# Kernel tuning notes

Hardware: AMD Instinct MI355X
Metric: run time of the kernel (lower is better)

## Reference

```python
import jax, jax.numpy as jnp
import numpy as np

B, N, C, H, W = 2, 6, 256, 56, 100
Q, E, NH = 900, 256, 8
EPS = 1e-5


def setup_inputs() -> dict:
    key = jax.random.key(0)
    ks = jax.random.split(key, 20)
    s = 0.02
    return {
        "image_features": jax.random.normal(ks[0], (B, N, C, H, W), jnp.float32),
        "lidar2img": jax.random.normal(ks[1], (B, N, 4, 4), jnp.float32),
        "query_table": jax.random.normal(ks[2], (Q, E), jnp.float32) * s,
        "ref_W": jax.random.normal(ks[3], (E, 3), jnp.float32) * s,
        "ref_b": jnp.zeros((3,), jnp.float32),
        "Wq": jax.random.normal(ks[4], (E, E), jnp.float32) * s,
        "bq": jnp.zeros((E,), jnp.float32),
        "Wk": jax.random.normal(ks[5], (E, E), jnp.float32) * s,
        "bk": jnp.zeros((E,), jnp.float32),
        "Wv": jax.random.normal(ks[6], (E, E), jnp.float32) * s,
        "bv": jnp.zeros((E,), jnp.float32),
        "Wo": jax.random.normal(ks[7], (E, E), jnp.float32) * s,
        "bo": jnp.zeros((E,), jnp.float32),
        "ln_g": jnp.ones((E,), jnp.float32),
        "ln_b": jnp.zeros((E,), jnp.float32),
        "box_W": jax.random.normal(ks[8], (E, 10), jnp.float32) * s,
        "box_b": jnp.zeros((10,), jnp.float32),
    }


def _grid_sample_bilinear(feats, grid):
    # feats: (M,C,H,W); grid: (M,P,2) in [-1,1]; align_corners=False, zero padding
    M, Cc, Hh, Ww = feats.shape
    gx, gy = grid[..., 0], grid[..., 1]
    x = ((gx + 1.0) * Ww - 1.0) * 0.5
    y = ((gy + 1.0) * Hh - 1.0) * 0.5
    x0 = jnp.floor(x); y0 = jnp.floor(y)
    wx1 = x - x0; wx0 = 1.0 - wx1
    wy1 = y - y0; wy0 = 1.0 - wy1
    midx = jnp.arange(M)[:, None]

    def gather(xi, yi):
        inb = (xi >= 0) & (xi < Ww) & (yi >= 0) & (yi < Hh)
        xi_c = jnp.clip(xi, 0, Ww - 1).astype(jnp.int32)
        yi_c = jnp.clip(yi, 0, Hh - 1).astype(jnp.int32)
        vals = feats[midx, :, yi_c, xi_c]  # (M,P,C)
        return vals * inb[..., None].astype(feats.dtype)

    out = (gather(x0, y0) * (wx0 * wy0)[..., None]
           + gather(x0 + 1, y0) * (wx1 * wy0)[..., None]
           + gather(x0, y0 + 1) * (wx0 * wy1)[..., None]
           + gather(x0 + 1, y0 + 1) * (wx1 * wy1)[..., None])
    return out  # (M,P,C)


def _layer_norm(x, g, b):
    mu = jnp.mean(x, -1, keepdims=True)
    var = jnp.mean((x - mu) ** 2, -1, keepdims=True)
    return (x - mu) * jax.lax.rsqrt(var + EPS) * g + b


def _forward(image_features, lidar2img, query_table, ref_W, ref_b,
             Wq, bq, Wk, bk, Wv, bv, Wo, bo, ln_g, ln_b, box_W, box_b):
    Bv = image_features.shape[0]
    qe = jnp.broadcast_to(query_table[None], (Bv, Q, E))  # (B,Q,E)

    # Step 1: reference points
    ref3d = jax.nn.sigmoid(qe @ ref_W + ref_b)  # (B,Q,3)

    # Step 2: project 3D -> 2D
    pts_h = jnp.concatenate([ref3d, jnp.ones_like(ref3d[..., :1])], -1)  # (B,Q,4)
    p2h = jnp.einsum('bnij,bqj->bnqi', lidar2img, pts_h)  # (B,N,Q,4)
    z = p2h[..., 2:3]
    pts2d = p2h[..., 0:2] / (jnp.abs(z) + 1e-5)  # (B,N,Q,2)
    zmask = (z > 1e-5)[..., 0]  # (B,N,Q)

    # Step 3: normalize + grid_sample + masked average
    gx = pts2d[..., 0] / (W - 1) * 2.0 - 1.0
    gy = pts2d[..., 1] / (H - 1) * 2.0 - 1.0
    grid = jnp.stack([gx, gy], -1).reshape(Bv * N, Q, 2)
    feats = image_features.reshape(Bv * N, C, H, W)
    samp = _grid_sample_bilinear(feats, grid).reshape(Bv, N, Q, C)
    samp = jnp.transpose(samp, (0, 2, 1, 3))  # (B,Q,N,C)

    valid = (gx > -1) & (gx < 1) & (gy > -1) & (gy < 1)  # (B,N,Q)
    final_mask = (zmask & valid).transpose(0, 2, 1)[..., None]  # (B,Q,N,1)
    samp = samp * final_mask.astype(samp.dtype)
    count = jnp.clip(final_mask.sum(2), 1, None).astype(samp.dtype)  # (B,Q,1)
    tgt = samp.sum(2) / count  # (B,Q,C)

    x = qe + tgt

    # self-attention (torch MultiheadAttention math)
    hd = E // NH
    q = (x @ Wq + bq).reshape(Bv, Q, NH, hd)
    k = (x @ Wk + bk).reshape(Bv, Q, NH, hd)
    v = (x @ Wv + bv).reshape(Bv, Q, NH, hd)
    att = jnp.einsum('bqhd,bkhd->bhqk', q, k) / jnp.sqrt(jnp.float32(hd))
    att = jax.nn.softmax(att, -1)
    o = jnp.einsum('bhqk,bkhd->bqhd', att, v).reshape(Bv, Q, E)
    x = o @ Wo + bo

    out = _layer_norm(x, ln_g, ln_b) @ box_W + box_b  # (B,Q,10)
    return out, ref3d


def reference(image_features, lidar2img, query_table, ref_W, ref_b,
              Wq, bq, Wk, bk, Wv, bv, Wo, bo, ln_g, ln_b, box_W, box_b):
    return _forward(image_features, lidar2img, query_table, ref_W, ref_b,
                    Wq, bq, Wk, bk, Wv, bv, Wo, bo, ln_g, ln_b, box_W, box_b)
```

## Files before the change

### kernel.cpp

```cpp
#include <hip/hip_runtime.h>
#include <math.h>

static constexpr int Bv  = 2;
static constexpr int Ncam= 6;
static constexpr int Cch = 256;
static constexpr int Hh  = 56;
static constexpr int Ww  = 100;
static constexpr int Pn  = Hh * Ww;
static constexpr int Qn  = 900;
static constexpr int En  = 256;
static constexpr int NH  = 8;
static constexpr int HD  = 32;

typedef _Float16 f16x8 __attribute__((ext_vector_type(8)));
typedef _Float16 f16x4 __attribute__((ext_vector_type(4)));
typedef float    f32x4 __attribute__((ext_vector_type(4)));

__global__ void wpack_kernel(const float* __restrict__ W0,
                             const float* __restrict__ W1,
                             const float* __restrict__ W2,
                             const float* __restrict__ W3,
                             _Float16* __restrict__ outp) {
    __shared__ float tile[32][33];
    int z = blockIdx.z;
    const float* src = (z == 0) ? W0 : (z == 1) ? W1 : (z == 2) ? W2 : W3;
    int k0 = blockIdx.x * 32, n0 = blockIdx.y * 32;
    int tx = threadIdx.x, ty = threadIdx.y;
    for (int i = 0; i < 32; i += 8)
        tile[ty + i][tx] = src[(size_t)(k0 + ty + i) * 256 + n0 + tx];
    __syncthreads();
    _Float16* dst = outp + (size_t)z * 256 * 256;
    for (int i = 0; i < 32; i += 8)
        dst[(size_t)(n0 + ty + i) * 256 + k0 + tx] = (_Float16)tile[tx][ty + i];
}

__global__ void ref_grid_kernel(const float* __restrict__ qt,
                                const float* __restrict__ refW,
                                const float* __restrict__ refb,
                                const float* __restrict__ l2i,
                                float* __restrict__ gridbuf,
                                float* __restrict__ out_ref3d) {
    int q = blockIdx.x;
    int t = threadIdx.x;
    float s0 = 0.f, s1 = 0.f, s2 = 0.f;
    for (int i = t; i < En; i += 64) {
        float a = qt[q * En + i];
        s0 += a * refW[i * 3 + 0];
        s1 += a * refW[i * 3 + 1];
        s2 += a * refW[i * 3 + 2];
    }
    for (int off = 32; off > 0; off >>= 1) {
        s0 += __shfl_down(s0, off);
        s1 += __shfl_down(s1, off);
        s2 += __shfl_down(s2, off);
    }
    __shared__ float r3[3];
    if (t == 0) {
        float v0 = 1.f / (1.f + expf(-(s0 + refb[0])));
        float v1 = 1.f / (1.f + expf(-(s1 + refb[1])));
        float v2 = 1.f / (1.f + expf(-(s2 + refb[2])));
        r3[0] = v0; r3[1] = v1; r3[2] = v2;
        out_ref3d[(size_t)(0 * Qn + q) * 3 + 0] = v0;
        out_ref3d[(size_t)(0 * Qn + q) * 3 + 1] = v1;
        out_ref3d[(size_t)(0 * Qn + q) * 3 + 2] = v2;
        out_ref3d[(size_t)(1 * Qn + q) * 3 + 0] = v0;
        out_ref3d[(size_t)(1 * Qn + q) * 3 + 1] = v1;
        out_ref3d[(size_t)(1 * Qn + q) * 3 + 2] = v2;
    }
    __syncthreads();
    if (t < Bv * Ncam) {
        int b = t / Ncam, n = t % Ncam;
        const float* M = l2i + (size_t)(b * Ncam + n) * 16;
        float p0 = M[0] * r3[0] + M[1] * r3[1] + M[2]  * r3[2] + M[3];
        float p1 = M[4] * r3[0] + M[5] * r3[1] + M[6]  * r3[2] + M[7];
        float z  = M[8] * r3[0] + M[9] * r3[1] + M[10] * r3[2] + M[11];
        float denom = fabsf(z) + 1e-5f;
        float px = p0 / denom, py = p1 / denom;
        float gx = px / (float)(Ww - 1) * 2.f - 1.f;
        float gy = py / (float)(Hh - 1) * 2.f - 1.f;
        bool zm = z > 1e-5f;
        bool valid = (gx > -1.f) && (gx < 1.f) && (gy > -1.f) && (gy < 1.f);
        float* g = gridbuf + ((size_t)(b * Ncam + n) * Qn + q) * 3;
        g[0] = gx; g[1] = gy; g[2] = (zm && valid) ? 1.f : 0.f;
    }
}

__global__ __launch_bounds__(256)
void feat_pack_kernel(const float* __restrict__ in, _Float16* __restrict__ outp) {
    __shared__ _Float16 tile[32][132];
    int m = blockIdx.z;
    int p0 = blockIdx.x * 128, c0 = blockIdx.y * 32;
    int t = threadIdx.x;
    {
        int p4 = (t & 31) * 4;
        int cc0 = t >> 5;
        for (int i = 0; i < 4; i++) {
            int cc = cc0 + i * 8;
            int p = p0 + p4;
            if (p < Pn) {
                float4 v = *(const float4*)&in[((size_t)m * Cch + c0 + cc) * Pn + p];
                f16x4 h = {(_Float16)v.x, (_Float16)v.y, (_Float16)v.z, (_Float16)v.w};
                *(f16x4*)&tile[cc][p4] = h;
            }
        }
    }
    __syncthreads();
    {
        int cg = (t & 7) * 4;
        int pr = t >> 3;
        for (int i = 0; i < 4; i++) {
            int pl = pr + i * 32;
            int p = p0 + pl;
            if (p < Pn) {
                f16x4 h = {tile[0][0], tile[0][0], tile[0][0], tile[0][0]};
                h.x = tile[cg + 0][pl];
                h.y = tile[cg + 1][pl];
                h.z = tile[cg + 2][pl];
                h.w = tile[cg + 3][pl];
                *(f16x4*)&outp[((size_t)m * Pn + p) * Cch + c0 + cg] = h;
            }
        }
    }
}

__device__ __forceinline__ float corner_val(const _Float16* __restrict__ base,
                                            int xi, int yi, int c) {
    if (xi < 0 || xi >= Ww || yi < 0 || yi >= Hh) return 0.f;
    return (float)base[((size_t)yi * Ww + xi) * Cch + c];
}

__global__ void sample_kernel(const _Float16* __restrict__ featsT,
                              const float* __restrict__ gridbuf,
                              const float* __restrict__ qt,
                              _Float16* __restrict__ xbuf) {
    int bq = blockIdx.x;
    int b = bq / Qn, q = bq % Qn;
    int c = threadIdx.x;
    float acc = 0.f, cnt = 0.f;
    for (int n = 0; n < Ncam; n++) {
        const float* g = gridbuf + ((size_t)(b * Ncam + n) * Qn + q) * 3;
        float gx = g[0], gy = g[1], msk = g[2];
        if (msk > 0.5f) {
            cnt += 1.f;
            float x = ((gx + 1.f) * (float)Ww - 1.f) * 0.5f;
            float y = ((gy + 1.f) * (float)Hh - 1.f) * 0.5f;
            float x0f = floorf(x), y0f = floorf(y);
            int x0 = (int)x0f, y0 = (int)y0f;
            float wx1 = x - x0f, wx0 = 1.f - wx1;
            float wy1 = y - y0f, wy0 = 1.f - wy1;
            int m = b * Ncam + n;
            const _Float16* base = featsT + (size_t)m * Pn * Cch;
            acc += corner_val(base, x0,     y0,     c) * (wx0 * wy0);
            acc += corner_val(base, x0 + 1, y0,     c) * (wx1 * wy0);
            acc += corner_val(base, x0,     y0 + 1, c) * (wx0 * wy1);
            acc += corner_val(base, x0 + 1, y0 + 1, c) * (wx1 * wy1);
        }
    }
    float tgt = acc / fmaxf(cnt, 1.f);
    xbuf[(size_t)bq * En + c] = (_Float16)(qt[q * En + c] + tgt);
}

__device__ __forceinline__ void mfma_gemm_body(const _Float16* __restrict__ A,
                                               const _Float16* __restrict__ Wt,
                                               const float* __restrict__ bias,
                                               _Float16* __restrict__ Cf16,
                                               float* __restrict__ Cf32,
                                               int M, int m0, int n0) {
    __shared__ _Float16 Ws[64][264];
    int t = threadIdx.x;
    int wave = t >> 6, lane = t & 63, quad = lane >> 4, col = lane & 15;
    {
        int row = t >> 5;
        int off = (t & 31) * 8;
        for (int i = 0; i < 8; i++)
            *(f16x8*)&Ws[row + i * 8][off] =
                *(const f16x8*)&Wt[(size_t)(n0 + row + i * 8) * 256 + off];
    }
    f16x8 af[8];
    int mrow = m0 + wave * 16 + col;
    if (mrow < M) {
        const _Float16* ap = A + (size_t)mrow * 256 + quad * 8;
        #pragma unroll
        for (int kc = 0; kc < 8; kc++) af[kc] = *(const f16x8*)(ap + kc * 32);
    } else {
        #pragma unroll
        for (int kc = 0; kc < 8; kc++)
            #pragma unroll
            for (int j = 0; j < 8; j++) af[kc][j] = (_Float16)0.f;
    }
    __syncthreads();
    f32x4 acc[4];
    #pragma unroll
    for (int nt = 0; nt < 4; nt++) { acc[nt][0]=0.f; acc[nt][1]=0.f; acc[nt][2]=0.f; acc[nt][3]=0.f; }
    #pragma unroll
    for (int nt = 0; nt < 4; nt++)
        #pragma unroll
        for (int kc = 0; kc < 8; kc++) {
            f16x8 bf = *(const f16x8*)&Ws[nt * 16 + col][kc * 32 + quad * 8];
            acc[nt] = __builtin_amdgcn_mfma_f32_16x16x32_f16(af[kc], bf, acc[nt], 0, 0, 0);
        }
    #pragma unroll
    for (int nt = 0; nt < 4; nt++) {
        int n = n0 + nt * 16 + col;
        float bv = bias[n];
        #pragma unroll
        for (int r = 0; r < 4; r++) {
            int m = m0 + wave * 16 + quad * 4 + r;
            if (m < M) {
                float v = acc[nt][r] + bv;
                if (Cf16) Cf16[(size_t)m * 256 + n] = (_Float16)v;
                else      Cf32[(size_t)m * 256 + n] = v;
            }
        }
    }
}

__global__ __launch_bounds__(256)
void qkv_mfma_kernel(const _Float16* __restrict__ A,
                     const _Float16* __restrict__ Wtall,
                     const float* __restrict__ bq, const float* __restrict__ bk,
                     const float* __restrict__ bv,
                     _Float16* __restrict__ qo, _Float16* __restrict__ ko,
                     _Float16* __restrict__ vo, int M) {
    const _Float16* Wt; const float* bias; _Float16* out;
    if (blockIdx.z == 0)      { Wt = Wtall;               bias = bq; out = qo; }
    else if (blockIdx.z == 1) { Wt = Wtall + 256 * 256;   bias = bk; out = ko; }
    else                      { Wt = Wtall + 2 * 256 * 256; bias = bv; out = vo; }
    mfma_gemm_body(A, Wt, bias, out, nullptr, M, blockIdx.x * 64, blockIdx.y * 64);
}

__global__ __launch_bounds__(256)
void wo_mfma_kernel(const _Float16* __restrict__ A,
                    const _Float16* __restrict__ Wtall,
                    const float* __restrict__ bo,
                    float* __restrict__ x2, int M) {
    mfma_gemm_body(A, Wtall + 3 * 256 * 256, bo, nullptr, x2, M,
                   blockIdx.x * 64, blockIdx.y * 64);
}

static constexpr int FTQ = 64;
static constexpr int FTK = 64;

__global__ __launch_bounds__(256)
void flash_attn_mfma_kernel(const _Float16* __restrict__ qbuf,
                            const _Float16* __restrict__ kbuf,
                            const _Float16* __restrict__ vbuf,
                            _Float16* __restrict__ obuf) {
    __shared__ _Float16 Ks[FTK][40];
    __shared__ _Float16 Vt[HD][72];
    __shared__ _Float16 Ps[4][16][72];

    int bh = blockIdx.y;
    int b = bh / NH, h = bh % NH;
    int m0 = blockIdx.x * FTQ;
    int t = threadIdx.x;
    int wave = t >> 6, lane = t & 63;
    int quad = lane >> 4, col = lane & 15;

    const float scale = 0.17677669529663687f;

    f16x8 qf;
    {
        int qrow = m0 + wave * 16 + col;
        if (qrow < Qn) {
            qf = *(const f16x8*)(qbuf + ((size_t)b * Qn + qrow) * En + h * HD + quad * 8);
        } else {
            #pragma unroll
            for (int j = 0; j < 8; j++) qf[j] = (_Float16)0.f;
        }
    }

    f32x4 o0 = {0.f, 0.f, 0.f, 0.f};
    f32x4 o1 = {0.f, 0.f, 0.f, 0.f};
    float mrow[4] = {-3e38f, -3e38f, -3e38f, -3e38f};
    float lrow[4] = {0.f, 0.f, 0.f, 0.f};

    int nstage = t >> 2;
    int kk4 = (t & 3) * 8;

    for (int n0 = 0; n0 < Qn; n0 += FTK) {
        {
            int ng = n0 + nstage;
            f16x8 kb, vb;
            if (ng < Qn) {
                kb = *(const f16x8*)(kbuf + ((size_t)b * Qn + ng) * En + h * HD + kk4);
                vb = *(const f16x8*)(vbuf + ((size_t)b * Qn + ng) * En + h * HD + kk4);
            } else {
                #pragma unroll
                for (int j = 0; j < 8; j++) { kb[j] = (_Float16)0.f; vb[j] = (_Float16)0.f; }
            }
            *(f16x8*)&Ks[nstage][kk4] = kb;
            #pragma unroll
            for (int j = 0; j < 8; j++) Vt[kk4 + j][nstage] = vb[j];
        }
        __syncthreads();

        f32x4 S[4];
        #pragma unroll
        for (int c = 0; c < 4; c++) {
            f16x8 kf = *(const f16x8*)&Ks[c * 16 + col][quad * 8];
            f32x4 z = {0.f, 0.f, 0.f, 0.f};
            S[c] = __builtin_amdgcn_mfma_f32_16x16x32_f16(qf, kf, z, 0, 0, 0);
            S[c] *= scale;
        }
        if (n0 + FTK > Qn) {
            #pragma unroll
            for (int c = 0; c < 4; c++) {
                if (n0 + c * 16 + col >= Qn) {
                    S[c][0] = -3e38f; S[c][1] = -3e38f; S[c][2] = -3e38f; S[c][3] = -3e38f;
                }
            }
        }

        float p[4][4];
        #pragma unroll
        for (int r = 0; r < 4; r++) {
            float mx = fmaxf(fmaxf(S[0][r], S[1][r]), fmaxf(S[2][r], S[3][r]));
            #pragma unroll
            for (int off = 8; off >= 1; off >>= 1)
                mx = fmaxf(mx, __shfl_xor(mx, off, 64));
            float mnew = fmaxf(mrow[r], mx);
            float alpha = __expf(mrow[r] - mnew);
            mrow[r] = mnew;
            float rs = 0.f;
            #pragma unroll
            for (int c = 0; c < 4; c++) {
                float pv = __expf(S[c][r] - mnew);
                p[c][r] = pv;
                rs += pv;
            }
            #pragma unroll
            for (int off = 8; off >= 1; off >>= 1)
                rs += __shfl_xor(rs, off, 64);
            lrow[r] = lrow[r] * alpha + rs;
            o0[r] *= alpha;
            o1[r] *= alpha;
        }

        #pragma unroll
        for (int c = 0; c < 4; c++)
            #pragma unroll
            for (int r = 0; r < 4; r++)
                Ps[wave][quad * 4 + r][c * 16 + col] = (_Float16)p[c][r];

        #pragma unroll
        for (int kc = 0; kc < 2; kc++) {
            f16x8 pf = *(const f16x8*)&Ps[wave][col][kc * 32 + quad * 8];
            f16x8 v0 = *(const f16x8*)&Vt[col][kc * 32 + quad * 8];
            f16x8 v1 = *(const f16x8*)&Vt[16 + col][kc * 32 + quad * 8];
            o0 = __builtin_amdgcn_mfma_f32_16x16x32_f16(pf, v0, o0, 0, 0, 0);
            o1 = __builtin_amdgcn_mfma_f32_16x16x32_f16(pf, v1, o1, 0, 0, 0);
        }
        __syncthreads();
    }

    #pragma unroll
    for (int r = 0; r < 4; r++) {
        int q = m0 + wave * 16 + quad * 4 + r;
        if (q < Qn) {
            float inv = 1.f / lrow[r];
            _Float16* op = obuf + ((size_t)b * Qn + q) * En + h * HD;
            op[col]      = (_Float16)(o0[r] * inv);
            op[16 + col] = (_Float16)(o1[r] * inv);
        }
    }
}

__global__ void ln_box_kernel(const float* __restrict__ x2,
                              const float* __restrict__ ln_g,
                              const float* __restrict__ ln_b,
                              const float* __restrict__ boxW,
                              const float* __restrict__ boxb,
                              float* __restrict__ outp) {
    __shared__ float red[256];
    __shared__ float yrow[En];
    __shared__ float pbox[16][10];
    int bq = blockIdx.x;
    int t = threadIdx.x;
    float acc = x2[(size_t)bq * En + t];
    red[t] = acc; __syncthreads();
    for (int s = 128; s > 0; s >>= 1) {
        if (t < s) red[t] += red[t + s];
        __syncthreads();
    }
    float mu = red[0] / (float)En;
    __syncthreads();
    float dx = acc - mu;
    red[t] = dx * dx; __syncthreads();
    for (int s = 128; s > 0; s >>= 1) {
        if (t < s) red[t] += red[t + s];
        __syncthreads();
    }
    float var = red[0] / (float)En;
    float y = dx * rsqrtf(var + 1e-5f) * ln_g[t] + ln_b[t];
    yrow[t] = y;
    __syncthreads();
    if (t < 160) {
        int j = t % 10, ch = t / 10;
        float p = 0.f;
        for (int k = ch * 16; k < ch * 16 + 16; k++)
            p += yrow[k] * boxW[(size_t)k * 10 + j];
        pbox[ch][j] = p;
    }
    __syncthreads();
    if (t < 10) {
        float o = boxb[t];
        for (int ch = 0; ch < 16; ch++) o += pbox[ch][t];
        outp[(size_t)bq * 10 + t] = o;
    }
}

extern "C" void kernel_launch(void* const* d_in, const int* in_sizes, int n_in,
                              void* d_out, int out_size, void* d_ws, size_t ws_size,
                              hipStream_t stream) {
    const float* image_features = (const float*)d_in[0];
    const float* lidar2img      = (const float*)d_in[1];
    const float* query_table    = (const float*)d_in[2];
    const float* ref_W          = (const float*)d_in[3];
    const float* ref_b          = (const float*)d_in[4];
    const float* Wq             = (const float*)d_in[5];
    const float* bq             = (const float*)d_in[6];
    const float* Wk             = (const float*)d_in[7];
    const float* bk             = (const float*)d_in[8];
    const float* Wv             = (const float*)d_in[9];
    const float* bv             = (const float*)d_in[10];
    const float* Wo             = (const float*)d_in[11];
    const float* bo             = (const float*)d_in[12];
    const float* ln_g           = (const float*)d_in[13];
    const float* ln_b           = (const float*)d_in[14];
    const float* box_W          = (const float*)d_in[15];
    const float* box_b          = (const float*)d_in[16];
    float* out = (float*)d_out;

    char* ws = (char*)d_ws;
    size_t off = 0;
    auto alloc = [&](size_t bytes) { char* p = ws + off; off += (bytes + 255) & ~size_t(255); return p; };
    float*     gridbuf = (float*)    alloc((size_t)Bv * Ncam * Qn * 3 * 4);
    _Float16*  featsT  = (_Float16*) alloc((size_t)Bv * Ncam * Pn * Cch * 2);
    _Float16*  xbuf    = (_Float16*) alloc((size_t)Bv * Qn * En * 2);
    _Float16*  qbuf    = (_Float16*) alloc((size_t)Bv * Qn * En * 2);
    _Float16*  kbuf    = (_Float16*) alloc((size_t)Bv * Qn * En * 2);
    _Float16*  vbuf    = (_Float16*) alloc((size_t)Bv * Qn * En * 2);
    _Float16*  obuf    = (_Float16*) alloc((size_t)Bv * Qn * En * 2);
    float*     x2buf   = (float*)    alloc((size_t)Bv * Qn * En * 4);
    _Float16*  Wtall   = (_Float16*) alloc((size_t)4 * 256 * 256 * 2);

    float* out_ref3d = out + (size_t)Bv * Qn * 10;
    int M = Bv * Qn;

    hipLaunchKernelGGL(wpack_kernel, dim3(8, 8, 4), dim3(32, 8), 0, stream,
                       Wq, Wk, Wv, Wo, Wtall);

    hipLaunchKernelGGL(ref_grid_kernel, dim3(Qn), dim3(64), 0, stream,
                       query_table, ref_W, ref_b, lidar2img, gridbuf, out_ref3d);

    hipLaunchKernelGGL(feat_pack_kernel,
                       dim3((Pn + 127) / 128, Cch / 32, Bv * Ncam), dim3(256),
                       0, stream, image_features, featsT);

    hipLaunchKernelGGL(sample_kernel, dim3(Bv * Qn), dim3(256), 0, stream,
                       featsT, gridbuf, query_table, xbuf);

    hipLaunchKernelGGL(qkv_mfma_kernel, dim3((M + 63) / 64, En / 64, 3), dim3(256),
                       0, stream, xbuf, Wtall, bq, bk, bv, qbuf, kbuf, vbuf, M);

    hipLaunchKernelGGL(flash_attn_mfma_kernel,
                       dim3((Qn + FTQ - 1) / FTQ, Bv * NH), dim3(256), 0, stream,
                       qbuf, kbuf, vbuf, obuf);

    hipLaunchKernelGGL(wo_mfma_kernel, dim3((M + 63) / 64, En / 64), dim3(256),
                       0, stream, obuf, Wtall, bo, x2buf, M);

    hipLaunchKernelGGL(ln_box_kernel, dim3(Bv * Qn), dim3(256), 0, stream,
                       x2buf, ln_g, ln_b, box_W, box_b, out);
}
```

Before: 185.0 us.

## Fuse prelude kernels, Wo GEMM with LayerNorm/box head; widen attention K tile

```diff
diff --git a/kernel.cpp b/kernel.cpp
--- a/kernel.cpp
+++ b/kernel.cpp
@@ -14,74 +14,72 @@
 
 typedef _Float16 f16x8 __attribute__((ext_vector_type(8)));
 typedef _Float16 f16x4 __attribute__((ext_vector_type(4)));
+typedef _Float16 f16x2 __attribute__((ext_vector_type(2)));
 typedef float    f32x4 __attribute__((ext_vector_type(4)));
 
-__global__ void wpack_kernel(const float* __restrict__ W0,
-                             const float* __restrict__ W1,
-                             const float* __restrict__ W2,
-                             const float* __restrict__ W3,
-                             _Float16* __restrict__ outp) {
-    __shared__ float tile[32][33];
-    int z = blockIdx.z;
-    const float* src = (z == 0) ? W0 : (z == 1) ? W1 : (z == 2) ? W2 : W3;
-    int k0 = blockIdx.x * 32, n0 = blockIdx.y * 32;
-    int tx = threadIdx.x, ty = threadIdx.y;
-    for (int i = 0; i < 32; i += 8)
-        tile[ty + i][tx] = src[(size_t)(k0 + ty + i) * 256 + n0 + tx];
-    __syncthreads();
-    _Float16* dst = outp + (size_t)z * 256 * 256;
-    for (int i = 0; i < 32; i += 8)
-        dst[(size_t)(n0 + ty + i) * 256 + k0 + tx] = (_Float16)tile[tx][ty + i];
-}
-
-__global__ void ref_grid_kernel(const float* __restrict__ qt,
-                                const float* __restrict__ refW,
-                                const float* __restrict__ refb,
-                                const float* __restrict__ l2i,
-                                float* __restrict__ gridbuf,
-                                float* __restrict__ out_ref3d) {
-    int q = blockIdx.x;
+__global__ __launch_bounds__(256)
+void prelude_kernel(const float* __restrict__ W0, const float* __restrict__ W1,
+                    const float* __restrict__ W2, const float* __restrict__ W3,
+                    _Float16* __restrict__ wt_out,
+                    const float* __restrict__ qt, const float* __restrict__ refW,
+                    const float* __restrict__ refb, const float* __restrict__ l2i,
+                    float* __restrict__ gridbuf, float* __restrict__ out_ref3d) {
+    int bid = blockIdx.x;
     int t = threadIdx.x;
-    float s0 = 0.f, s1 = 0.f, s2 = 0.f;
-    for (int i = t; i < En; i += 64) {
-        float a = qt[q * En + i];
-        s0 += a * refW[i * 3 + 0];
-        s1 += a * refW[i * 3 + 1];
-        s2 += a * refW[i * 3 + 2];
-    }
-    for (int off = 32; off > 0; off >>= 1) {
-        s0 += __shfl_down(s0, off);
-        s1 += __shfl_down(s1, off);
-        s2 += __shfl_down(s2, off);
-    }
-    __shared__ float r3[3];
-    if (t == 0) {
-        float v0 = 1.f / (1.f + expf(-(s0 + refb[0])));
-        float v1 = 1.f / (1.f + expf(-(s1 + refb[1])));
-        float v2 = 1.f / (1.f + expf(-(s2 + refb[2])));
-        r3[0] = v0; r3[1] = v1; r3[2] = v2;
-        out_ref3d[(size_t)(0 * Qn + q) * 3 + 0] = v0;
-        out_ref3d[(size_t)(0 * Qn + q) * 3 + 1] = v1;
-        out_ref3d[(size_t)(0 * Qn + q) * 3 + 2] = v2;
-        out_ref3d[(size_t)(1 * Qn + q) * 3 + 0] = v0;
-        out_ref3d[(size_t)(1 * Qn + q) * 3 + 1] = v1;
-        out_ref3d[(size_t)(1 * Qn + q) * 3 + 2] = v2;
-    }
-    __syncthreads();
-    if (t < Bv * Ncam) {
-        int b = t / Ncam, n = t % Ncam;
-        const float* M = l2i + (size_t)(b * Ncam + n) * 16;
-        float p0 = M[0] * r3[0] + M[1] * r3[1] + M[2]  * r3[2] + M[3];
-        float p1 = M[4] * r3[0] + M[5] * r3[1] + M[6]  * r3[2] + M[7];
-        float z  = M[8] * r3[0] + M[9] * r3[1] + M[10] * r3[2] + M[11];
-        float denom = fabsf(z) + 1e-5f;
-        float px = p0 / denom, py = p1 / denom;
-        float gx = px / (float)(Ww - 1) * 2.f - 1.f;
-        float gy = py / (float)(Hh - 1) * 2.f - 1.f;
-        bool zm = z > 1e-5f;
-        bool valid = (gx > -1.f) && (gx < 1.f) && (gy > -1.f) && (gy < 1.f);
-        float* g = gridbuf + ((size_t)(b * Ncam + n) * Qn + q) * 3;
-        g[0] = gx; g[1] = gy; g[2] = (zm && valid) ? 1.f : 0.f;
+    if (bid < 256) {
+        __shared__ float tile[32][33];
+        int z = bid >> 6, rem = bid & 63;
+        const float* src = (z == 0) ? W0 : (z == 1) ? W1 : (z == 2) ? W2 : W3;
+        int k0 = (rem & 7) * 32, n0 = (rem >> 3) * 32;
+        int tx = t & 31, ty = t >> 5;
+        for (int i = 0; i < 32; i += 8)
+            tile[ty + i][tx] = src[(size_t)(k0 + ty + i) * 256 + n0 + tx];
+        __syncthreads();
+        _Float16* dst = wt_out + (size_t)z * 256 * 256;
+        for (int i = 0; i < 32; i += 8)
+            dst[(size_t)(n0 + ty + i) * 256 + k0 + tx] = (_Float16)tile[tx][ty + i];
+    } else {
+        int wave = t >> 6, lane = t & 63;
+        int q = (bid - 256) * 4 + wave;
+        float s0 = 0.f, s1 = 0.f, s2 = 0.f;
+        for (int i = lane; i < En; i += 64) {
+            float a = qt[q * En + i];
+            s0 += a * refW[i * 3 + 0];
+            s1 += a * refW[i * 3 + 1];
+            s2 += a * refW[i * 3 + 2];
+        }
+        for (int off = 32; off > 0; off >>= 1) {
+            s0 += __shfl_down(s0, off);
+            s1 += __shfl_down(s1, off);
+            s2 += __shfl_down(s2, off);
+        }
+        s0 = __shfl(s0, 0); s1 = __shfl(s1, 0); s2 = __shfl(s2, 0);
+        float v0 = 1.f / (1.f + __expf(-(s0 + refb[0])));
+        float v1 = 1.f / (1.f + __expf(-(s1 + refb[1])));
+        float v2 = 1.f / (1.f + __expf(-(s2 + refb[2])));
+        if (lane == 0) {
+            out_ref3d[(size_t)q * 3 + 0] = v0;
+            out_ref3d[(size_t)q * 3 + 1] = v1;
+            out_ref3d[(size_t)q * 3 + 2] = v2;
+            out_ref3d[(size_t)(Qn + q) * 3 + 0] = v0;
+            out_ref3d[(size_t)(Qn + q) * 3 + 1] = v1;
+            out_ref3d[(size_t)(Qn + q) * 3 + 2] = v2;
+        }
+        if (lane < Bv * Ncam) {
+            int b = lane / Ncam, n = lane % Ncam;
+            const float* M = l2i + (size_t)(b * Ncam + n) * 16;
+            float p0 = M[0] * v0 + M[1] * v1 + M[2]  * v2 + M[3];
+            float p1 = M[4] * v0 + M[5] * v1 + M[6]  * v2 + M[7];
+            float z  = M[8] * v0 + M[9] * v1 + M[10] * v2 + M[11];
+            float denom = fabsf(z) + 1e-5f;
+            float px = p0 / denom, py = p1 / denom;
+            float gx = px / (float)(Ww - 1) * 2.f - 1.f;
+            float gy = py / (float)(Hh - 1) * 2.f - 1.f;
+            bool zm = z > 1e-5f;
+            bool valid = (gx > -1.f) && (gx < 1.f) && (gy > -1.f) && (gy < 1.f);
+            float* g = gridbuf + ((size_t)(b * Ncam + n) * Qn + q) * 3;
+            g[0] = gx; g[1] = gy; g[2] = (zm && valid) ? 1.f : 0.f;
+        }
     }
 }
 
@@ -112,7 +110,7 @@
             int pl = pr + i * 32;
             int p = p0 + pl;
             if (p < Pn) {
-                f16x4 h = {tile[0][0], tile[0][0], tile[0][0], tile[0][0]};
+                f16x4 h;
                 h.x = tile[cg + 0][pl];
                 h.y = tile[cg + 1][pl];
                 h.z = tile[cg + 2][pl];
@@ -123,20 +121,25 @@
     }
 }
 
-__device__ __forceinline__ float corner_val(const _Float16* __restrict__ base,
-                                            int xi, int yi, int c) {
-    if (xi < 0 || xi >= Ww || yi < 0 || yi >= Hh) return 0.f;
-    return (float)base[((size_t)yi * Ww + xi) * Cch + c];
-}
-
-__global__ void sample_kernel(const _Float16* __restrict__ featsT,
-                              const float* __restrict__ gridbuf,
-                              const float* __restrict__ qt,
-                              _Float16* __restrict__ xbuf) {
-    int bq = blockIdx.x;
+__device__ __forceinline__ void corner_acc2(const _Float16* __restrict__ base,
+                                            int xi, int yi, int ch, float w,
+                                            float& a0, float& a1) {
+    if (xi < 0 || xi >= Ww || yi < 0 || yi >= Hh) return;
+    f16x2 v = *(const f16x2*)&base[((size_t)yi * Ww + xi) * Cch + ch];
+    a0 += (float)v.x * w;
+    a1 += (float)v.y * w;
+}
+
+__global__ __launch_bounds__(256)
+void sample_kernel(const _Float16* __restrict__ featsT,
+                   const float* __restrict__ gridbuf,
+                   const float* __restrict__ qt,
+                   _Float16* __restrict__ xbuf) {
+    int t = threadIdx.x;
+    int bq = blockIdx.x * 2 + (t >> 7);
     int b = bq / Qn, q = bq % Qn;
-    int c = threadIdx.x;
-    float acc = 0.f, cnt = 0.f;
+    int ch = (t & 127) * 2;
+    float a0 = 0.f, a1 = 0.f, cnt = 0.f;
     for (int n = 0; n < Ncam; n++) {
         const float* g = gridbuf + ((size_t)(b * Ncam + n) * Qn + q) * 3;
         float gx = g[0], gy = g[1], msk = g[2];
@@ -148,23 +151,25 @@
             int x0 = (int)x0f, y0 = (int)y0f;
             float wx1 = x - x0f, wx0 = 1.f - wx1;
             float wy1 = y - y0f, wy0 = 1.f - wy1;
-            int m = b * Ncam + n;
-            const _Float16* base = featsT + (size_t)m * Pn * Cch;
-            acc += corner_val(base, x0,     y0,     c) * (wx0 * wy0);
-            acc += corner_val(base, x0 + 1, y0,     c) * (wx1 * wy0);
-            acc += corner_val(base, x0,     y0 + 1, c) * (wx0 * wy1);
-            acc += corner_val(base, x0 + 1, y0 + 1, c) * (wx1 * wy1);
-        }
-    }
-    float tgt = acc / fmaxf(cnt, 1.f);
-    xbuf[(size_t)bq * En + c] = (_Float16)(qt[q * En + c] + tgt);
+            const _Float16* base = featsT + (size_t)(b * Ncam + n) * Pn * Cch;
+            corner_acc2(base, x0,     y0,     ch, wx0 * wy0, a0, a1);
+            corner_acc2(base, x0 + 1, y0,     ch, wx1 * wy0, a0, a1);
+            corner_acc2(base, x0,     y0 + 1, ch, wx0 * wy1, a0, a1);
+            corner_acc2(base, x0 + 1, y0 + 1, ch, wx1 * wy1, a0, a1);
+        }
+    }
+    float inv = 1.f / fmaxf(cnt, 1.f);
+    float2 qv = *(const float2*)&qt[(size_t)q * En + ch];
+    f16x2 o;
+    o.x = (_Float16)(qv.x + a0 * inv);
+    o.y = (_Float16)(qv.y + a1 * inv);
+    *(f16x2*)&xbuf[(size_t)bq * En + ch] = o;
 }
 
 __device__ __forceinline__ void mfma_gemm_body(const _Float16* __restrict__ A,
                                                const _Float16* __restrict__ Wt,
                                                const float* __restrict__ bias,
                                                _Float16* __restrict__ Cf16,
-                                               float* __restrict__ Cf32,
                                                int M, int m0, int n0) {
     __shared__ _Float16 Ws[64][264];
     int t = threadIdx.x;
@@ -206,11 +211,7 @@
         #pragma unroll
         for (int r = 0; r < 4; r++) {
             int m = m0 + wave * 16 + quad * 4 + r;
-            if (m < M) {
-                float v = acc[nt][r] + bv;
-                if (Cf16) Cf16[(size_t)m * 256 + n] = (_Float16)v;
-                else      Cf32[(size_t)m * 256 + n] = v;
-            }
+            if (m < M) Cf16[(size_t)m * 256 + n] = (_Float16)(acc[nt][r] + bv);
         }
     }
 }
@@ -223,23 +224,14 @@
                      _Float16* __restrict__ qo, _Float16* __restrict__ ko,
                      _Float16* __restrict__ vo, int M) {
     const _Float16* Wt; const float* bias; _Float16* out;
-    if (blockIdx.z == 0)      { Wt = Wtall;               bias = bq; out = qo; }
-    else if (blockIdx.z == 1) { Wt = Wtall + 256 * 256;   bias = bk; out = ko; }
+    if (blockIdx.z == 0)      { Wt = Wtall;                 bias = bq; out = qo; }
+    else if (blockIdx.z == 1) { Wt = Wtall + 256 * 256;     bias = bk; out = ko; }
     else                      { Wt = Wtall + 2 * 256 * 256; bias = bv; out = vo; }
-    mfma_gemm_body(A, Wt, bias, out, nullptr, M, blockIdx.x * 64, blockIdx.y * 64);
-}
-
-__global__ __launch_bounds__(256)
-void wo_mfma_kernel(const _Float16* __restrict__ A,
-                    const _Float16* __restrict__ Wtall,
-                    const float* __restrict__ bo,
-                    float* __restrict__ x2, int M) {
-    mfma_gemm_body(A, Wtall + 3 * 256 * 256, bo, nullptr, x2, M,
-                   blockIdx.x * 64, blockIdx.y * 64);
+    mfma_gemm_body(A, Wt, bias, out, M, blockIdx.x * 64, blockIdx.y * 64);
 }
 
 static constexpr int FTQ = 64;
-static constexpr int FTK = 64;
+static constexpr int FTK = 128;
 
 __global__ __launch_bounds__(256)
 void flash_attn_mfma_kernel(const _Float16* __restrict__ qbuf,
@@ -247,8 +239,8 @@
                             const _Float16* __restrict__ vbuf,
                             _Float16* __restrict__ obuf) {
     __shared__ _Float16 Ks[FTK][40];
-    __shared__ _Float16 Vt[HD][72];
-    __shared__ _Float16 Ps[4][16][72];
+    __shared__ _Float16 Vt[HD][FTK + 8];
+    __shared__ _Float16 Ps[4][16][FTK + 8];
 
     int bh = blockIdx.y;
     int b = bh / NH, h = bh % NH;
@@ -275,29 +267,36 @@
     float mrow[4] = {-3e38f, -3e38f, -3e38f, -3e38f};
     float lrow[4] = {0.f, 0.f, 0.f, 0.f};
 
-    int nstage = t >> 2;
-    int kk4 = (t & 3) * 8;
+    int nstage = t >> 1;
+    int koff = (t & 1) * 16;
 
     for (int n0 = 0; n0 < Qn; n0 += FTK) {
         {
             int ng = n0 + nstage;
-            f16x8 kb, vb;
+            f16x8 k0v, k1v, v0v, v1v;
             if (ng < Qn) {
-                kb = *(const f16x8*)(kbuf + ((size_t)b * Qn + ng) * En + h * HD + kk4);
-                vb = *(const f16x8*)(vbuf + ((size_t)b * Qn + ng) * En + h * HD + kk4);
+                const _Float16* kp = kbuf + ((size_t)b * Qn + ng) * En + h * HD + koff;
+                const _Float16* vp = vbuf + ((size_t)b * Qn + ng) * En + h * HD + koff;
+                k0v = *(const f16x8*)kp;       k1v = *(const f16x8*)(kp + 8);
+                v0v = *(const f16x8*)vp;       v1v = *(const f16x8*)(vp + 8);
             } else {
                 #pragma unroll
-                for (int j = 0; j < 8; j++) { kb[j] = (_Float16)0.f; vb[j] = (_Float16)0.f; }
-            }
-            *(f16x8*)&Ks[nstage][kk4] = kb;
-            #pragma unroll
-            for (int j = 0; j < 8; j++) Vt[kk4 + j][nstage] = vb[j];
+                for (int j = 0; j < 8; j++) { k0v[j]=(_Float16)0.f; k1v[j]=(_Float16)0.f;
+                                              v0v[j]=(_Float16)0.f; v1v[j]=(_Float16)0.f; }
+            }
+            *(f16x8*)&Ks[nstage][koff]     = k0v;
+            *(f16x8*)&Ks[nstage][koff + 8] = k1v;
+            #pragma unroll
+            for (int j = 0; j < 8; j++) {
+                Vt[koff + j][nstage]     = v0v[j];
+                Vt[koff + 8 + j][nstage] = v1v[j];
+            }
         }
         __syncthreads();
 
-        f32x4 S[4];
-        #pragma unroll
-        for (int c = 0; c < 4; c++) {
+        f32x4 S[8];
+        #pragma unroll
+        for (int c = 0; c < 8; c++) {
             f16x8 kf = *(const f16x8*)&Ks[c * 16 + col][quad * 8];
             f32x4 z = {0.f, 0.f, 0.f, 0.f};
             S[c] = __builtin_amdgcn_mfma_f32_16x16x32_f16(qf, kf, z, 0, 0, 0);
@@ -305,17 +304,19 @@
         }
         if (n0 + FTK > Qn) {
             #pragma unroll
-            for (int c = 0; c < 4; c++) {
+            for (int c = 0; c < 8; c++) {
                 if (n0 + c * 16 + col >= Qn) {
                     S[c][0] = -3e38f; S[c][1] = -3e38f; S[c][2] = -3e38f; S[c][3] = -3e38f;
                 }
             }
         }
 
-        float p[4][4];
+        float p[8][4];
         #pragma unroll
         for (int r = 0; r < 4; r++) {
-            float mx = fmaxf(fmaxf(S[0][r], S[1][r]), fmaxf(S[2][r], S[3][r]));
+            float mx = S[0][r];
+            #pragma unroll
+            for (int c = 1; c < 8; c++) mx = fmaxf(mx, S[c][r]);
             #pragma unroll
             for (int off = 8; off >= 1; off >>= 1)
                 mx = fmaxf(mx, __shfl_xor(mx, off, 64));
@@ -324,7 +325,7 @@
             mrow[r] = mnew;
             float rs = 0.f;
             #pragma unroll
-            for (int c = 0; c < 4; c++) {
+            for (int c = 0; c < 8; c++) {
                 float pv = __expf(S[c][r] - mnew);
                 p[c][r] = pv;
                 rs += pv;
@@ -338,13 +339,13 @@
         }
 
         #pragma unroll
-        for (int c = 0; c < 4; c++)
+        for (int c = 0; c < 8; c++)
             #pragma unroll
             for (int r = 0; r < 4; r++)
                 Ps[wave][quad * 4 + r][c * 16 + col] = (_Float16)p[c][r];
 
         #pragma unroll
-        for (int kc = 0; kc < 2; kc++) {
+        for (int kc = 0; kc < 4; kc++) {
             f16x8 pf = *(const f16x8*)&Ps[wave][col][kc * 32 + quad * 8];
             f16x8 v0 = *(const f16x8*)&Vt[col][kc * 32 + quad * 8];
             f16x8 v1 = *(const f16x8*)&Vt[16 + col][kc * 32 + quad * 8];
@@ -366,47 +367,106 @@
     }
 }
 
-__global__ void ln_box_kernel(const float* __restrict__ x2,
-                              const float* __restrict__ ln_g,
-                              const float* __restrict__ ln_b,
-                              const float* __restrict__ boxW,
-                              const float* __restrict__ boxb,
-                              float* __restrict__ outp) {
-    __shared__ float red[256];
-    __shared__ float yrow[En];
-    __shared__ float pbox[16][10];
-    int bq = blockIdx.x;
+__global__ __launch_bounds__(256)
+void wo_ln_box_kernel(const _Float16* __restrict__ A,
+                      const _Float16* __restrict__ Wtall,
+                      const float* __restrict__ bo,
+                      const float* __restrict__ ln_g,
+                      const float* __restrict__ ln_b,
+                      const float* __restrict__ boxW,
+                      const float* __restrict__ boxb,
+                      float* __restrict__ outp, int M) {
+    __shared__ __align__(16) char smem[64 * 272 * 2];
+    _Float16 (*Ws)[264] = (_Float16(*)[264])smem;
+    _Float16 (*yL)[272] = (_Float16(*)[272])smem;
+
+    const _Float16* Wt = Wtall + 3 * 256 * 256;
     int t = threadIdx.x;
-    float acc = x2[(size_t)bq * En + t];
-    red[t] = acc; __syncthreads();
-    for (int s = 128; s > 0; s >>= 1) {
-        if (t < s) red[t] += red[t + s];
+    int wave = t >> 6, lane = t & 63, quad = lane >> 4, col = lane & 15;
+    int m0 = blockIdx.x * 64;
+
+    f16x8 af[8];
+    int mrow = m0 + wave * 16 + col;
+    if (mrow < M) {
+        const _Float16* ap = A + (size_t)mrow * 256 + quad * 8;
+        #pragma unroll
+        for (int kc = 0; kc < 8; kc++) af[kc] = *(const f16x8*)(ap + kc * 32);
+    } else {
+        #pragma unroll
+        for (int kc = 0; kc < 8; kc++)
+            #pragma unroll
+            for (int j = 0; j < 8; j++) af[kc][j] = (_Float16)0.f;
+    }
+
+    f32x4 acc[16];
+    #pragma unroll
+    for (int i = 0; i < 16; i++) { acc[i][0]=0.f; acc[i][1]=0.f; acc[i][2]=0.f; acc[i][3]=0.f; }
+
+    for (int g = 0; g < 4; g++) {
         __syncthreads();
-    }
-    float mu = red[0] / (float)En;
+        {
+            int row = t >> 5;
+            int off = (t & 31) * 8;
+            for (int i = 0; i < 8; i++)
+                *(f16x8*)&Ws[row + i * 8][off] =
+                    *(const f16x8*)&Wt[(size_t)(g * 64 + row + i * 8) * 256 + off];
+        }
+        __syncthreads();
+        #pragma unroll
+        for (int nt2 = 0; nt2 < 4; nt2++)
+            #pragma unroll
+            for (int kc = 0; kc < 8; kc++) {
+                f16x8 bf = *(const f16x8*)&Ws[nt2 * 16 + col][kc * 32 + quad * 8];
+                acc[g * 4 + nt2] =
+                    __builtin_amdgcn_mfma_f32_16x16x32_f16(af[kc], bf, acc[g * 4 + nt2], 0, 0, 0);
+            }
+    }
     __syncthreads();
-    float dx = acc - mu;
-    red[t] = dx * dx; __syncthreads();
-    for (int s = 128; s > 0; s >>= 1) {
-        if (t < s) red[t] += red[t + s];
-        __syncthreads();
-    }
-    float var = red[0] / (float)En;
-    float y = dx * rsqrtf(var + 1e-5f) * ln_g[t] + ln_b[t];
-    yrow[t] = y;
+
+    #pragma unroll
+    for (int r = 0; r < 4; r++) {
+        float v[16];
+        float sum = 0.f;
+        #pragma unroll
+        for (int nt = 0; nt < 16; nt++) {
+            v[nt] = acc[nt][r] + bo[nt * 16 + col];
+            sum += v[nt];
+        }
+        sum += __shfl_xor(sum, 1, 64);
+        sum += __shfl_xor(sum, 2, 64);
+        sum += __shfl_xor(sum, 4, 64);
+        sum += __shfl_xor(sum, 8, 64);
+        float mu = sum * (1.f / 256.f);
+        float sq = 0.f;
+        #pragma unroll
+        for (int nt = 0; nt < 16; nt++) { float d = v[nt] - mu; sq += d * d; }
+        sq += __shfl_xor(sq, 1, 64);
+        sq += __shfl_xor(sq, 2, 64);
+        sq += __shfl_xor(sq, 4, 64);
+        sq += __shfl_xor(sq, 8, 64);
+        float rstd = rsqrtf(sq * (1.f / 256.f) + 1e-5f);
+        int lrow = wave * 16 + quad * 4 + r;
+        #pragma unroll
+        for (int nt = 0; nt < 16; nt++) {
+            int n = nt * 16 + col;
+            yL[lrow][n] = (_Float16)((v[nt] - mu) * rstd * ln_g[n] + ln_b[n]);
+        }
+    }
     __syncthreads();
-    if (t < 160) {
-        int j = t % 10, ch = t / 10;
-        float p = 0.f;
-        for (int k = ch * 16; k < ch * 16 + 16; k++)
-            p += yrow[k] * boxW[(size_t)k * 10 + j];
-        pbox[ch][j] = p;
-    }
-    __syncthreads();
-    if (t < 10) {
-        float o = boxb[t];
-        for (int ch = 0; ch < 16; ch++) o += pbox[ch][t];
-        outp[(size_t)bq * 10 + t] = o;
+
+    for (int idx = t; idx < 640; idx += 256) {
+        int row = idx / 10, j = idx % 10;
+        int m = m0 + row;
+        if (m < M) {
+            float s = boxb[j];
+            for (int k8 = 0; k8 < 32; k8++) {
+                f16x8 y8 = *(const f16x8*)&yL[row][k8 * 8];
+                #pragma unroll
+                for (int u = 0; u < 8; u++)
+                    s += (float)y8[u] * boxW[(size_t)(k8 * 8 + u) * 10 + j];
+            }
+            outp[(size_t)m * 10 + j] = s;
+        }
     }
 }
 
@@ -442,23 +502,20 @@
     _Float16*  kbuf    = (_Float16*) alloc((size_t)Bv * Qn * En * 2);
     _Float16*  vbuf    = (_Float16*) alloc((size_t)Bv * Qn * En * 2);
     _Float16*  obuf    = (_Float16*) alloc((size_t)Bv * Qn * En * 2);
-    float*     x2buf   = (float*)    alloc((size_t)Bv * Qn * En * 4);
     _Float16*  Wtall   = (_Float16*) alloc((size_t)4 * 256 * 256 * 2);
 
     float* out_ref3d = out + (size_t)Bv * Qn * 10;
     int M = Bv * Qn;
 
-    hipLaunchKernelGGL(wpack_kernel, dim3(8, 8, 4), dim3(32, 8), 0, stream,
-                       Wq, Wk, Wv, Wo, Wtall);
-
-    hipLaunchKernelGGL(ref_grid_kernel, dim3(Qn), dim3(64), 0, stream,
+    hipLaunchKernelGGL(prelude_kernel, dim3(256 + 225), dim3(256), 0, stream,
+                       Wq, Wk, Wv, Wo, Wtall,
                        query_table, ref_W, ref_b, lidar2img, gridbuf, out_ref3d);
 
     hipLaunchKernelGGL(feat_pack_kernel,
                        dim3((Pn + 127) / 128, Cch / 32, Bv * Ncam), dim3(256),
                        0, stream, image_features, featsT);
 
-    hipLaunchKernelGGL(sample_kernel, dim3(Bv * Qn), dim3(256), 0, stream,
+    hipLaunchKernelGGL(sample_kernel, dim3(Bv * Qn / 2), dim3(256), 0, stream,
                        featsT, gridbuf, query_table, xbuf);
 
     hipLaunchKernelGGL(qkv_mfma_kernel, dim3((M + 63) / 64, En / 64, 3), dim3(256),
@@ -468,9 +525,6 @@
                        dim3((Qn + FTQ - 1) / FTQ, Bv * NH), dim3(256), 0, stream,
                        qbuf, kbuf, vbuf, obuf);
 
-    hipLaunchKernelGGL(wo_mfma_kernel, dim3((M + 63) / 64, En / 64), dim3(256),
-                       0, stream, obuf, Wtall, bo, x2buf, M);
-
-    hipLaunchKernelGGL(ln_box_kernel, dim3(Bv * Qn), dim3(256), 0, stream,
-                       x2buf, ln_g, ln_b, box_W, box_b, out);
-}
+    hipLaunchKernelGGL(wo_ln_box_kernel, dim3((M + 63) / 64), dim3(256), 0, stream,
+                       obuf, Wtall, bo, ln_g, ln_b, box_W, box_b, out, M);
+}
```

New measurement: 200.1 us. +8.1%, slower.

## Fuse prelude kernels, vectorize sampling, shrink attention query tile

Applied to the files above, without the earlier changes.

```diff
diff --git a/kernel.cpp b/kernel.cpp
--- a/kernel.cpp
+++ b/kernel.cpp
@@ -14,74 +14,72 @@
 
 typedef _Float16 f16x8 __attribute__((ext_vector_type(8)));
 typedef _Float16 f16x4 __attribute__((ext_vector_type(4)));
+typedef _Float16 f16x2 __attribute__((ext_vector_type(2)));
 typedef float    f32x4 __attribute__((ext_vector_type(4)));
 
-__global__ void wpack_kernel(const float* __restrict__ W0,
-                             const float* __restrict__ W1,
-                             const float* __restrict__ W2,
-                             const float* __restrict__ W3,
-                             _Float16* __restrict__ outp) {
-    __shared__ float tile[32][33];
-    int z = blockIdx.z;
-    const float* src = (z == 0) ? W0 : (z == 1) ? W1 : (z == 2) ? W2 : W3;
-    int k0 = blockIdx.x * 32, n0 = blockIdx.y * 32;
-    int tx = threadIdx.x, ty = threadIdx.y;
-    for (int i = 0; i < 32; i += 8)
-        tile[ty + i][tx] = src[(size_t)(k0 + ty + i) * 256 + n0 + tx];
-    __syncthreads();
-    _Float16* dst = outp + (size_t)z * 256 * 256;
-    for (int i = 0; i < 32; i += 8)
-        dst[(size_t)(n0 + ty + i) * 256 + k0 + tx] = (_Float16)tile[tx][ty + i];
-}
-
-__global__ void ref_grid_kernel(const float* __restrict__ qt,
-                                const float* __restrict__ refW,
-                                const float* __restrict__ refb,
-                                const float* __restrict__ l2i,
-                                float* __restrict__ gridbuf,
-                                float* __restrict__ out_ref3d) {
-    int q = blockIdx.x;
-    int t = threadIdx.x;
-    float s0 = 0.f, s1 = 0.f, s2 = 0.f;
-    for (int i = t; i < En; i += 64) {
-        float a = qt[q * En + i];
-        s0 += a * refW[i * 3 + 0];
-        s1 += a * refW[i * 3 + 1];
-        s2 += a * refW[i * 3 + 2];
-    }
-    for (int off = 32; off > 0; off >>= 1) {
-        s0 += __shfl_down(s0, off);
-        s1 += __shfl_down(s1, off);
-        s2 += __shfl_down(s2, off);
-    }
-    __shared__ float r3[3];
-    if (t == 0) {
-        float v0 = 1.f / (1.f + expf(-(s0 + refb[0])));
-        float v1 = 1.f / (1.f + expf(-(s1 + refb[1])));
-        float v2 = 1.f / (1.f + expf(-(s2 + refb[2])));
-        r3[0] = v0; r3[1] = v1; r3[2] = v2;
-        out_ref3d[(size_t)(0 * Qn + q) * 3 + 0] = v0;
-        out_ref3d[(size_t)(0 * Qn + q) * 3 + 1] = v1;
-        out_ref3d[(size_t)(0 * Qn + q) * 3 + 2] = v2;
-        out_ref3d[(size_t)(1 * Qn + q) * 3 + 0] = v0;
-        out_ref3d[(size_t)(1 * Qn + q) * 3 + 1] = v1;
-        out_ref3d[(size_t)(1 * Qn + q) * 3 + 2] = v2;
-    }
-    __syncthreads();
-    if (t < Bv * Ncam) {
-        int b = t / Ncam, n = t % Ncam;
-        const float* M = l2i + (size_t)(b * Ncam + n) * 16;
-        float p0 = M[0] * r3[0] + M[1] * r3[1] + M[2]  * r3[2] + M[3];
-        float p1 = M[4] * r3[0] + M[5] * r3[1] + M[6]  * r3[2] + M[7];
-        float z  = M[8] * r3[0] + M[9] * r3[1] + M[10] * r3[2] + M[11];
-        float denom = fabsf(z) + 1e-5f;
-        float px = p0 / denom, py = p1 / denom;
-        float gx = px / (float)(Ww - 1) * 2.f - 1.f;
-        float gy = py / (float)(Hh - 1) * 2.f - 1.f;
-        bool zm = z > 1e-5f;
-        bool valid = (gx > -1.f) && (gx < 1.f) && (gy > -1.f) && (gy < 1.f);
-        float* g = gridbuf + ((size_t)(b * Ncam + n) * Qn + q) * 3;
-        g[0] = gx; g[1] = gy; g[2] = (zm && valid) ? 1.f : 0.f;
+__global__ __launch_bounds__(256)
+void prelude_kernel(const float* __restrict__ W0, const float* __restrict__ W1,
+                    const float* __restrict__ W2, const float* __restrict__ W3,
+                    _Float16* __restrict__ wt_out,
+                    const float* __restrict__ qt, const float* __restrict__ refW,
+                    const float* __restrict__ refb, const float* __restrict__ l2i,
+                    float* __restrict__ gridbuf, float* __restrict__ out_ref3d) {
+    int bid = blockIdx.x;
+    int t = threadIdx.x;
+    if (bid < 256) {
+        __shared__ float tile[32][33];
+        int z = bid >> 6, rem = bid & 63;
+        const float* src = (z == 0) ? W0 : (z == 1) ? W1 : (z == 2) ? W2 : W3;
+        int k0 = (rem & 7) * 32, n0 = (rem >> 3) * 32;
+        int tx = t & 31, ty = t >> 5;
+        for (int i = 0; i < 32; i += 8)
+            tile[ty + i][tx] = src[(size_t)(k0 + ty + i) * 256 + n0 + tx];
+        __syncthreads();
+        _Float16* dst = wt_out + (size_t)z * 256 * 256;
+        for (int i = 0; i < 32; i += 8)
+            dst[(size_t)(n0 + ty + i) * 256 + k0 + tx] = (_Float16)tile[tx][ty + i];
+    } else {
+        int wave = t >> 6, lane = t & 63;
+        int q = (bid - 256) * 4 + wave;
+        float s0 = 0.f, s1 = 0.f, s2 = 0.f;
+        for (int i = lane; i < En; i += 64) {
+            float a = qt[q * En + i];
+            s0 += a * refW[i * 3 + 0];
+            s1 += a * refW[i * 3 + 1];
+            s2 += a * refW[i * 3 + 2];
+        }
+        for (int off = 32; off > 0; off >>= 1) {
+            s0 += __shfl_down(s0, off);
+            s1 += __shfl_down(s1, off);
+            s2 += __shfl_down(s2, off);
+        }
+        s0 = __shfl(s0, 0); s1 = __shfl(s1, 0); s2 = __shfl(s2, 0);
+        float v0 = 1.f / (1.f + __expf(-(s0 + refb[0])));
+        float v1 = 1.f / (1.f + __expf(-(s1 + refb[1])));
+        float v2 = 1.f / (1.f + __expf(-(s2 + refb[2])));
+        if (lane == 0) {
+            out_ref3d[(size_t)q * 3 + 0] = v0;
+            out_ref3d[(size_t)q * 3 + 1] = v1;
+            out_ref3d[(size_t)q * 3 + 2] = v2;
+            out_ref3d[(size_t)(Qn + q) * 3 + 0] = v0;
+            out_ref3d[(size_t)(Qn + q) * 3 + 1] = v1;
+            out_ref3d[(size_t)(Qn + q) * 3 + 2] = v2;
+        }
+        if (lane < Bv * Ncam) {
+            int b = lane / Ncam, n = lane % Ncam;
+            const float* M = l2i + (size_t)(b * Ncam + n) * 16;
+            float p0 = M[0] * v0 + M[1] * v1 + M[2]  * v2 + M[3];
+            float p1 = M[4] * v0 + M[5] * v1 + M[6]  * v2 + M[7];
+            float z  = M[8] * v0 + M[9] * v1 + M[10] * v2 + M[11];
+            float denom = fabsf(z) + 1e-5f;
+            float px = p0 / denom, py = p1 / denom;
+            float gx = px / (float)(Ww - 1) * 2.f - 1.f;
+            float gy = py / (float)(Hh - 1) * 2.f - 1.f;
+            bool zm = z > 1e-5f;
+            bool valid = (gx > -1.f) && (gx < 1.f) && (gy > -1.f) && (gy < 1.f);
+            float* g = gridbuf + ((size_t)(b * Ncam + n) * Qn + q) * 3;
+            g[0] = gx; g[1] = gy; g[2] = (zm && valid) ? 1.f : 0.f;
+        }
     }
 }
 
@@ -112,7 +110,7 @@
             int pl = pr + i * 32;
             int p = p0 + pl;
             if (p < Pn) {
-                f16x4 h = {tile[0][0], tile[0][0], tile[0][0], tile[0][0]};
+                f16x4 h;
                 h.x = tile[cg + 0][pl];
                 h.y = tile[cg + 1][pl];
                 h.z = tile[cg + 2][pl];
@@ -123,20 +121,25 @@
     }
 }
 
-__device__ __forceinline__ float corner_val(const _Float16* __restrict__ base,
-                                            int xi, int yi, int c) {
-    if (xi < 0 || xi >= Ww || yi < 0 || yi >= Hh) return 0.f;
-    return (float)base[((size_t)yi * Ww + xi) * Cch + c];
-}
-
-__global__ void sample_kernel(const _Float16* __restrict__ featsT,
-                              const float* __restrict__ gridbuf,
-                              const float* __restrict__ qt,
-                              _Float16* __restrict__ xbuf) {
-    int bq = blockIdx.x;
+__device__ __forceinline__ void corner_acc2(const _Float16* __restrict__ base,
+                                            int xi, int yi, int ch, float w,
+                                            float& a0, float& a1) {
+    if (xi < 0 || xi >= Ww || yi < 0 || yi >= Hh) return;
+    f16x2 v = *(const f16x2*)&base[((size_t)yi * Ww + xi) * Cch + ch];
+    a0 += (float)v.x * w;
+    a1 += (float)v.y * w;
+}
+
+__global__ __launch_bounds__(256)
+void sample_kernel(const _Float16* __restrict__ featsT,
+                   const float* __restrict__ gridbuf,
+                   const float* __restrict__ qt,
+                   _Float16* __restrict__ xbuf) {
+    int t = threadIdx.x;
+    int bq = blockIdx.x * 2 + (t >> 7);
     int b = bq / Qn, q = bq % Qn;
-    int c = threadIdx.x;
-    float acc = 0.f, cnt = 0.f;
+    int ch = (t & 127) * 2;
+    float a0 = 0.f, a1 = 0.f, cnt = 0.f;
     for (int n = 0; n < Ncam; n++) {
         const float* g = gridbuf + ((size_t)(b * Ncam + n) * Qn + q) * 3;
         float gx = g[0], gy = g[1], msk = g[2];
@@ -148,16 +151,19 @@
             int x0 = (int)x0f, y0 = (int)y0f;
             float wx1 = x - x0f, wx0 = 1.f - wx1;
             float wy1 = y - y0f, wy0 = 1.f - wy1;
-            int m = b * Ncam + n;
-            const _Float16* base = featsT + (size_t)m * Pn * Cch;
-            acc += corner_val(base, x0,     y0,     c) * (wx0 * wy0);
-            acc += corner_val(base, x0 + 1, y0,     c) * (wx1 * wy0);
-            acc += corner_val(base, x0,     y0 + 1, c) * (wx0 * wy1);
-            acc += corner_val(base, x0 + 1, y0 + 1, c) * (wx1 * wy1);
-        }
-    }
-    float tgt = acc / fmaxf(cnt, 1.f);
-    xbuf[(size_t)bq * En + c] = (_Float16)(qt[q * En + c] + tgt);
+            const _Float16* base = featsT + (size_t)(b * Ncam + n) * Pn * Cch;
+            corner_acc2(base, x0,     y0,     ch, wx0 * wy0, a0, a1);
+            corner_acc2(base, x0 + 1, y0,     ch, wx1 * wy0, a0, a1);
+            corner_acc2(base, x0,     y0 + 1, ch, wx0 * wy1, a0, a1);
+            corner_acc2(base, x0 + 1, y0 + 1, ch, wx1 * wy1, a0, a1);
+        }
+    }
+    float inv = 1.f / fmaxf(cnt, 1.f);
+    float2 qv = *(const float2*)&qt[(size_t)q * En + ch];
+    f16x2 o;
+    o.x = (_Float16)(qv.x + a0 * inv);
+    o.y = (_Float16)(qv.y + a1 * inv);
+    *(f16x2*)&xbuf[(size_t)bq * En + ch] = o;
 }
 
 __device__ __forceinline__ void mfma_gemm_body(const _Float16* __restrict__ A,
@@ -223,8 +229,8 @@
                      _Float16* __restrict__ qo, _Float16* __restrict__ ko,
                      _Float16* __restrict__ vo, int M) {
     const _Float16* Wt; const float* bias; _Float16* out;
-    if (blockIdx.z == 0)      { Wt = Wtall;               bias = bq; out = qo; }
-    else if (blockIdx.z == 1) { Wt = Wtall + 256 * 256;   bias = bk; out = ko; }
+    if (blockIdx.z == 0)      { Wt = Wtall;                 bias = bq; out = qo; }
+    else if (blockIdx.z == 1) { Wt = Wtall + 256 * 256;     bias = bk; out = ko; }
     else                      { Wt = Wtall + 2 * 256 * 256; bias = bv; out = vo; }
     mfma_gemm_body(A, Wt, bias, out, nullptr, M, blockIdx.x * 64, blockIdx.y * 64);
 }
@@ -238,17 +244,17 @@
                    blockIdx.x * 64, blockIdx.y * 64);
 }
 
-static constexpr int FTQ = 64;
+static constexpr int FTQ = 32;
 static constexpr int FTK = 64;
 
-__global__ __launch_bounds__(256)
+__global__ __launch_bounds__(128)
 void flash_attn_mfma_kernel(const _Float16* __restrict__ qbuf,
                             const _Float16* __restrict__ kbuf,
                             const _Float16* __restrict__ vbuf,
                             _Float16* __restrict__ obuf) {
     __shared__ _Float16 Ks[FTK][40];
     __shared__ _Float16 Vt[HD][72];
-    __shared__ _Float16 Ps[4][16][72];
+    __shared__ _Float16 Ps[2][16][72];
 
     int bh = blockIdx.y;
     int b = bh / NH, h = bh % NH;
@@ -275,23 +281,30 @@
     float mrow[4] = {-3e38f, -3e38f, -3e38f, -3e38f};
     float lrow[4] = {0.f, 0.f, 0.f, 0.f};
 
-    int nstage = t >> 2;
-    int kk4 = (t & 3) * 8;
+    int nstage = t >> 1;
+    int koff = (t & 1) * 16;
 
     for (int n0 = 0; n0 < Qn; n0 += FTK) {
         {
             int ng = n0 + nstage;
-            f16x8 kb, vb;
+            f16x8 k0v, k1v, v0v, v1v;
             if (ng < Qn) {
-                kb = *(const f16x8*)(kbuf + ((size_t)b * Qn + ng) * En + h * HD + kk4);
-                vb = *(const f16x8*)(vbuf + ((size_t)b * Qn + ng) * En + h * HD + kk4);
+                const _Float16* kp = kbuf + ((size_t)b * Qn + ng) * En + h * HD + koff;
+                const _Float16* vp = vbuf + ((size_t)b * Qn + ng) * En + h * HD + koff;
+                k0v = *(const f16x8*)kp;  k1v = *(const f16x8*)(kp + 8);
+                v0v = *(const f16x8*)vp;  v1v = *(const f16x8*)(vp + 8);
             } else {
                 #pragma unroll
-                for (int j = 0; j < 8; j++) { kb[j] = (_Float16)0.f; vb[j] = (_Float16)0.f; }
-            }
-            *(f16x8*)&Ks[nstage][kk4] = kb;
-            #pragma unroll
-            for (int j = 0; j < 8; j++) Vt[kk4 + j][nstage] = vb[j];
+                for (int j = 0; j < 8; j++) { k0v[j]=(_Float16)0.f; k1v[j]=(_Float16)0.f;
+                                              v0v[j]=(_Float16)0.f; v1v[j]=(_Float16)0.f; }
+            }
+            *(f16x8*)&Ks[nstage][koff]     = k0v;
+            *(f16x8*)&Ks[nstage][koff + 8] = k1v;
+            #pragma unroll
+            for (int j = 0; j < 8; j++) {
+                Vt[koff + j][nstage]     = v0v[j];
+                Vt[koff + 8 + j][nstage] = v1v[j];
+            }
         }
         __syncthreads();
 
@@ -448,24 +461,22 @@
     float* out_ref3d = out + (size_t)Bv * Qn * 10;
     int M = Bv * Qn;
 
-    hipLaunchKernelGGL(wpack_kernel, dim3(8, 8, 4), dim3(32, 8), 0, stream,
-                       Wq, Wk, Wv, Wo, Wtall);
-
-    hipLaunchKernelGGL(ref_grid_kernel, dim3(Qn), dim3(64), 0, stream,
+    hipLaunchKernelGGL(prelude_kernel, dim3(256 + 225), dim3(256), 0, stream,
+                       Wq, Wk, Wv, Wo, Wtall,
                        query_table, ref_W, ref_b, lidar2img, gridbuf, out_ref3d);
 
     hipLaunchKernelGGL(feat_pack_kernel,
                        dim3((Pn + 127) / 128, Cch / 32, Bv * Ncam), dim3(256),
                        0, stream, image_features, featsT);
 
-    hipLaunchKernelGGL(sample_kernel, dim3(Bv * Qn), dim3(256), 0, stream,
+    hipLaunchKernelGGL(sample_kernel, dim3(Bv * Qn / 2), dim3(256), 0, stream,
                        featsT, gridbuf, query_table, xbuf);
 
     hipLaunchKernelGGL(qkv_mfma_kernel, dim3((M + 63) / 64, En / 64, 3), dim3(256),
                        0, stream, xbuf, Wtall, bq, bk, bv, qbuf, kbuf, vbuf, M);
 
     hipLaunchKernelGGL(flash_attn_mfma_kernel,
-                       dim3((Qn + FTQ - 1) / FTQ, Bv * NH), dim3(256), 0, stream,
+                       dim3((Qn + FTQ - 1) / FTQ, Bv * NH), dim3(128), 0, stream,
                        qbuf, kbuf, vbuf, obuf);
 
     hipLaunchKernelGGL(wo_mfma_kernel, dim3((M + 63) / 64, En / 64), dim3(256),
```

New measurement: 185.8 us. No clear change (+0.4%).
